# Kernel tuning notes

Measured on AMD Instinct MI355X. Metric: run time of the kernel, lower is better.

The kernel has to match this reference:

```python
import jax, jax.numpy as jnp
import numpy as np

N = 100000       # num nodes
E = 3200000      # num edges
F_IN = 32        # num_node_features
F_EDGE = 16      # num_edge_features
H = 27           # hidden_dim
OUT = 1          # output_dim


def setup_inputs() -> dict:
    key = jax.random.key(0)
    ks = jax.random.split(key, 12)
    inp = {
        "x": jax.random.normal(ks[0], (N, F_IN), dtype=jnp.float32),
        "edge_index": jax.random.randint(ks[1], (2, E), 0, N, dtype=jnp.int64),
        "edge_attr": jax.random.normal(ks[2], (E, F_EDGE), dtype=jnp.float32),
        # GCNConv layer params (PyG uses weight [in, out] applied as x @ W)
        "W1": jax.random.normal(ks[3], (F_IN, H), dtype=jnp.float32) * (1.0 / np.sqrt(F_IN)),
        "b1": jnp.zeros((H,), dtype=jnp.float32),
        "W2": jax.random.normal(ks[4], (H, H), dtype=jnp.float32) * (1.0 / np.sqrt(H)),
        "b2": jnp.zeros((H,), dtype=jnp.float32),
        # edge MLP
        "ew1": jax.random.normal(ks[5], (F_EDGE, H), dtype=jnp.float32) * (1.0 / np.sqrt(F_EDGE)),
        "eb1": jnp.zeros((H,), dtype=jnp.float32),
        "ew2": jax.random.normal(ks[6], (H, H), dtype=jnp.float32) * (1.0 / np.sqrt(H)),
        "eb2": jnp.zeros((H,), dtype=jnp.float32),
        # final edge head: in = 2*H + H = 3*H
        "fcw": jax.random.normal(ks[7], (3 * H, OUT), dtype=jnp.float32) * (1.0 / np.sqrt(3 * H)),
        "fcb": jnp.zeros((OUT,), dtype=jnp.float32),
    }
    return inp


def gcn_conv(x, edge_index, W, b):
    # PyG GCNConv with add_self_loops=True, symmetric normalization.
    row, col = edge_index[0], edge_index[1]
    loops = jnp.arange(N, dtype=edge_index.dtype)
    row_sl = jnp.concatenate([row, loops])  # sources
    col_sl = jnp.concatenate([col, loops])  # targets
    # degree computed on target nodes (edge weights = 1)
    deg = jax.ops.segment_sum(jnp.ones_like(col_sl, dtype=x.dtype), col_sl, num_segments=N)
    dinv = jnp.where(deg > 0, jax.lax.rsqrt(deg), 0.0)
    norm = dinv[row_sl] * dinv[col_sl]  # [E+N]
    h = x @ W  # [N, H]
    msg = h[row_sl] * norm[:, None]  # gather + scale
    out = jax.ops.segment_sum(msg, col_sl, num_segments=N)  # scatter-add
    return out + b


def reference(x, edge_index, edge_attr, W1, b1, W2, b2, ew1, eb1, ew2, eb2, fcw, fcb):
    h = jax.nn.relu(gcn_conv(x, edge_index, W1, b1))
    # dropout is identity in eval mode (training=False)
    h = gcn_conv(h, edge_index, W2, b2)
    ef = jax.nn.relu(edge_attr @ ew1 + eb1) @ ew2 + eb2  # [E, H]
    row, col = edge_index[0], edge_index[1]
    emb = jnp.concatenate([h[row], h[col], ef], axis=1)  # [E, 3H]
    pred = (emb @ fcw + fcb).squeeze()  # [E]
    return pred
```

## Files before the change

kernel.cpp:

```cpp
#include <hip/hip_runtime.h>

#define N_NODES 100000
#define N_EDGES 3200000
#define F_IN 32
#define F_EDGE 16
#define H 27
#define PAD 32
#define NB_NODES 391
#define NBUCK 391
#define BCAP 9216
#define CHUNK 12500

__global__ __launch_bounds__(256) void k_initcur(int* __restrict__ cursor) {
    int i = blockIdx.x * 256 + threadIdx.x;
    if (i < NBUCK) cursor[i] = i * BCAP;
}

__global__ __launch_bounds__(1024) void k_bin(const int* __restrict__ ei,
                                              int* __restrict__ cursor,
                                              int* __restrict__ binned) {
    __shared__ int stage[CHUNK];
    __shared__ int hist[NBUCK];
    __shared__ int bstart[NBUCK];
    __shared__ int gbase[NBUCK];
    __shared__ int scanbuf[512];
    int tid = threadIdx.x;
    long long cs = (long long)blockIdx.x * CHUNK;

    for (int i = tid; i < NBUCK; i += 1024) hist[i] = 0;
    __syncthreads();

    int pk[13], bk[13], rk[13];
#pragma unroll
    for (int i = 0; i < 13; i++) {
        int j = tid + i * 1024;
        bk[i] = -1;
        if (j < CHUNK) {
            int e = (int)(cs + j);
            int r = ei[e];
            int c = ei[N_EDGES + e];
            int b = c >> 8;
            pk[i] = (r << 8) | (c & 255);
            bk[i] = b;
            rk[i] = atomicAdd(&hist[b], 1);
        }
    }
    __syncthreads();

    if (tid < 512) scanbuf[tid] = (tid < NBUCK) ? hist[tid] : 0;
    __syncthreads();
    for (int off = 1; off < 512; off <<= 1) {
        int v = 0;
        if (tid < 512 && tid >= off) v = scanbuf[tid - off];
        __syncthreads();
        if (tid < 512) scanbuf[tid] += v;
        __syncthreads();
    }
    if (tid < NBUCK) {
        bstart[tid] = scanbuf[tid] - hist[tid];
        gbase[tid] = (hist[tid] > 0) ? atomicAdd(&cursor[tid], hist[tid]) : 0;
    }
    __syncthreads();

#pragma unroll
    for (int i = 0; i < 13; i++) {
        if (bk[i] >= 0) stage[bstart[bk[i]] + rk[i]] = pk[i];
    }
    __syncthreads();

    for (int j = tid; j < CHUNK; j += 1024) {
        int lo = 0, hi = NBUCK - 1;
        while (lo < hi) {
            int mid = (lo + hi + 1) >> 1;
            if (bstart[mid] <= j) lo = mid; else hi = mid - 1;
        }
        binned[gbase[lo] + (j - bstart[lo])] = stage[j];
    }
}

__global__ __launch_bounds__(512) void k_bscan(const int* __restrict__ cursor,
                                               int* __restrict__ bbase,
                                               int* __restrict__ ptr) {
    __shared__ int sb[512];
    int tid = threadIdx.x;
    int cnt = (tid < NBUCK) ? (cursor[tid] - tid * BCAP) : 0;
    sb[tid] = cnt;
    __syncthreads();
    for (int off = 1; off < 512; off <<= 1) {
        int t = (tid >= off) ? sb[tid - off] : 0;
        __syncthreads();
        sb[tid] += t;
        __syncthreads();
    }
    if (tid < NBUCK) bbase[tid] = sb[tid] - cnt;
    if (tid == NBUCK - 1) ptr[N_NODES] = sb[tid];
}

__global__ __launch_bounds__(256) void k_bin2(const int* __restrict__ cursor,
                                              const int* __restrict__ binned,
                                              const int* __restrict__ bbase,
                                              int* __restrict__ ptr,
                                              int* __restrict__ csr,
                                              float* __restrict__ dinv) {
    __shared__ int hist[256];
    __shared__ int offs[256];
    __shared__ int stage[BCAP];
    int b = blockIdx.x, tid = threadIdx.x;
    hist[tid] = 0;
    __syncthreads();
    int base = b * BCAP;
    int cnt = cursor[b] - base;
    int gb = bbase[b];

    int recs[36], rks[36];
#pragma unroll
    for (int i = 0; i < 36; i++) {
        int j = tid + i * 256;
        recs[i] = -1;
        if (j < cnt) {
            int rec = binned[base + j];
            recs[i] = rec;
            rks[i] = atomicAdd(&hist[rec & 255], 1);
        }
    }
    __syncthreads();

    int v = hist[tid];
    offs[tid] = v;
    __syncthreads();
    for (int off = 1; off < 256; off <<= 1) {
        int t = (tid >= off) ? offs[tid - off] : 0;
        __syncthreads();
        offs[tid] += t;
        __syncthreads();
    }
    int excl = offs[tid] - v;
    int n = b * 256 + tid;
    if (n < N_NODES) {
        ptr[n] = gb + excl;
        dinv[n] = rsqrtf((float)(v + 1));
    }
    __syncthreads();
    offs[tid] = excl;
    __syncthreads();

#pragma unroll
    for (int i = 0; i < 36; i++) {
        if (recs[i] >= 0) stage[offs[recs[i] & 255] + rks[i]] = recs[i] >> 8;
    }
    __syncthreads();
    for (int j = tid; j < cnt; j += 256) csr[gb + j] = stage[j];
}

__global__ __launch_bounds__(256) void k_l1pre(const float* __restrict__ x,
                                               const float* __restrict__ W1,
                                               const float* __restrict__ dinv,
                                               float* __restrict__ bufA) {
    __shared__ float w[F_IN * H];
    for (int i = threadIdx.x; i < F_IN * H; i += 256) w[i] = W1[i];
    __syncthreads();
    int n = blockIdx.x * 256 + threadIdx.x;
    if (n >= N_NODES) return;

    float xv[F_IN];
    const float4* xp = (const float4*)(x + (long long)n * F_IN);
#pragma unroll
    for (int j = 0; j < F_IN / 4; j++) {
        float4 v = xp[j];
        xv[4 * j] = v.x; xv[4 * j + 1] = v.y; xv[4 * j + 2] = v.z; xv[4 * j + 3] = v.w;
    }
    float di = dinv[n];
    long long base = (long long)n * PAD;
#pragma unroll
    for (int j = 0; j < H; j++) {
        float acc = 0.f;
#pragma unroll
        for (int k = 0; k < F_IN; k++) acc += xv[k] * w[k * H + j];
        bufA[base + j] = acc * di;
    }
}

__global__ __launch_bounds__(256) void k_gather_post(const int* __restrict__ ptr,
                                                     const int* __restrict__ csr,
                                                     const float* __restrict__ bufA,
                                                     const float* __restrict__ W2,
                                                     const float* __restrict__ b1,
                                                     const float* __restrict__ fcw,
                                                     const float* __restrict__ dinv,
                                                     float2* __restrict__ s01) {
    __shared__ float w[H * H];
    __shared__ float bs[H], f0[H], f1[H];
    for (int i = threadIdx.x; i < H * H; i += 256) w[i] = W2[i];
    if (threadIdx.x < H) {
        bs[threadIdx.x] = b1[threadIdx.x];
        f0[threadIdx.x] = fcw[threadIdx.x];
        f1[threadIdx.x] = fcw[H + threadIdx.x];
    }
    __syncthreads();

    int g = blockIdx.x * 256 + threadIdx.x;
    int n = g >> 5;
    int lane = g & 31;
    if (n >= N_NODES) return;
    int sub = lane >> 3;
    int q = lane & 7;
    int p0 = ptr[n], p1 = ptr[n + 1];

    float4 a0 = make_float4(0.f, 0.f, 0.f, 0.f);
    float4 a1 = make_float4(0.f, 0.f, 0.f, 0.f);
    int i = p0;
    while (i < p1) {
        int m = p1 - i; if (m > 32) m = 32;
        int idx = (lane < m) ? csr[i + lane] : 0;
        for (int jj = 0; jj < m; jj += 8) {
            int e0 = jj + sub;
            int e1 = jj + 4 + sub;
            int r0 = __shfl(idx, e0, 32);
            int r1 = __shfl(idx, e1, 32);
            float4 v0 = ((const float4*)(bufA + (long long)r0 * PAD))[q];
            float4 v1 = ((const float4*)(bufA + (long long)r1 * PAD))[q];
            if (e0 < m) { a0.x += v0.x; a0.y += v0.y; a0.z += v0.z; a0.w += v0.w; }
            if (e1 < m) { a1.x += v1.x; a1.y += v1.y; a1.z += v1.z; a1.w += v1.w; }
        }
        i += m;
    }
    a0.x += a1.x; a0.y += a1.y; a0.z += a1.z; a0.w += a1.w;

    a0.x += __shfl_xor(a0.x, 8, 32);
    a0.y += __shfl_xor(a0.y, 8, 32);
    a0.z += __shfl_xor(a0.z, 8, 32);
    a0.w += __shfl_xor(a0.w, 8, 32);
    a0.x += __shfl_xor(a0.x, 16, 32);
    a0.y += __shfl_xor(a0.y, 16, 32);
    a0.z += __shfl_xor(a0.z, 16, 32);
    a0.w += __shfl_xor(a0.w, 16, 32);

    float4 sv = ((const float4*)(bufA + (long long)n * PAD))[q];
    a0.x += sv.x; a0.y += sv.y; a0.z += sv.z; a0.w += sv.w;

    int src = lane >> 2;
    float t0 = __shfl(a0.x, src, 32);
    float t1 = __shfl(a0.y, src, 32);
    float t2 = __shfl(a0.z, src, 32);
    float t3 = __shfl(a0.w, src, 32);
    int c = lane & 3;
    float acc = (c == 0) ? t0 : (c == 1) ? t1 : (c == 2) ? t2 : t3;

    float di = dinv[n];
    float o1 = 0.f;
    if (lane < H) {
        float t = bs[lane] + di * acc;
        o1 = t > 0.f ? t : 0.f;
    }
    float gj = 0.f;
#pragma unroll
    for (int k = 0; k < H; k++) {
        float ok = __shfl(o1, k, 32);
        if (lane < H) gj += ok * w[k * H + lane];
    }
    float t0h = 0.f, t1h = 0.f;
    if (lane < H) {
        float gd = gj * di;
        t0h = gd * f0[lane];
        t1h = gd * f1[lane];
    }
#pragma unroll
    for (int off = 16; off > 0; off >>= 1) {
        t0h += __shfl_xor(t0h, off, 32);
        t1h += __shfl_xor(t1h, off, 32);
    }
    if (lane == 0) s01[n] = make_float2(t0h, t1h);
}

__global__ void k_prep(const float* __restrict__ ew2,
                       const float* __restrict__ eb2,
                       const float* __restrict__ b2,
                       const float* __restrict__ fcw,
                       const float* __restrict__ fcb,
                       float* __restrict__ vbuf) {
    int k = threadIdx.x;
    if (k < H) {
        float acc = 0.f;
#pragma unroll
        for (int j = 0; j < H; j++) acc += ew2[k * H + j] * fcw[2 * H + j];
        vbuf[k] = acc;
    } else if (k == H) {
        float acc = fcb[0];
#pragma unroll
        for (int j = 0; j < H; j++) acc += eb2[j] * fcw[2 * H + j];
        vbuf[H] = acc;
    } else if (k == H + 1) {
        float acc = 0.f;
#pragma unroll
        for (int j = 0; j < H; j++) acc += b2[j] * fcw[j];
        vbuf[H + 1] = acc;
    } else if (k == H + 2) {
        float acc = 0.f;
#pragma unroll
        for (int j = 0; j < H; j++) acc += b2[j] * fcw[H + j];
        vbuf[H + 2] = acc;
    }
}

__global__ __launch_bounds__(256) void k_pull2(const int* __restrict__ ptr,
                                               const int* __restrict__ csr,
                                               const float2* __restrict__ s01,
                                               const float* __restrict__ dinv,
                                               const float* __restrict__ vbuf,
                                               float* __restrict__ pr,
                                               float* __restrict__ pc) {
    int g = blockIdx.x * 256 + threadIdx.x;
    int n = g >> 5;
    int lane = g & 31;
    if (n >= N_NODES) return;
    int p0 = ptr[n], p1 = ptr[n + 1];

    float a0 = 0.f, a1 = 0.f;
    for (int i = p0 + lane; i < p1; i += 32) {
        float2 s = s01[csr[i]];
        a0 += s.x;
        a1 += s.y;
    }
#pragma unroll
    for (int off = 16; off > 0; off >>= 1) {
        a0 += __shfl_down(a0, off, 32);
        a1 += __shfl_down(a1, off, 32);
    }
    if (lane == 0) {
        float2 ss = s01[n];
        float di = dinv[n];
        pr[n] = vbuf[H + 1] + di * (a0 + ss.x);
        pc[n] = vbuf[H + 2] + di * (a1 + ss.y);
    }
}

__global__ __launch_bounds__(256) void k_edge_final(const int* __restrict__ ei,
                                                    const float* __restrict__ ea,
                                                    const float* __restrict__ ew1,
                                                    const float* __restrict__ eb1,
                                                    const float* __restrict__ vbuf,
                                                    const float* __restrict__ pr,
                                                    const float* __restrict__ pc,
                                                    float* __restrict__ out) {
    __shared__ float w1t[H * F_EDGE];
    __shared__ float2 bv[H];
    __shared__ float c0s;
    for (int i = threadIdx.x; i < H * F_EDGE; i += 256) {
        int k = i >> 4, m = i & 15;
        w1t[i] = ew1[m * H + k];
    }
    if (threadIdx.x < H) bv[threadIdx.x] = make_float2(eb1[threadIdx.x], vbuf[threadIdx.x]);
    if (threadIdx.x == 0) c0s = vbuf[H];
    __syncthreads();

    long long t = (long long)blockIdx.x * 256 + threadIdx.x;
    long long e0 = t * 2;
    if (e0 >= N_EDGES) return;

    int2 rr = *(const int2*)(ei + e0);
    int2 cc = *(const int2*)(ei + N_EDGES + e0);
    float g0 = pr[rr.x];
    float g1 = pr[rr.y];
    float h0 = pc[cc.x];
    float h1 = pc[cc.y];

    float a[2][F_EDGE];
#pragma unroll
    for (int i = 0; i < 2; i++) {
        const float4* p = (const float4*)(ea + (e0 + i) * F_EDGE);
#pragma unroll
        for (int j = 0; j < F_EDGE / 4; j++) {
            float4 v = p[j];
            a[i][4 * j] = v.x; a[i][4 * j + 1] = v.y; a[i][4 * j + 2] = v.z; a[i][4 * j + 3] = v.w;
        }
    }

    float c0 = c0s;
    float acc0 = c0, acc1 = c0;
    const float4* w1v = (const float4*)w1t;
#pragma unroll
    for (int k = 0; k < H; k++) {
        float4 wa = w1v[k * 4 + 0];
        float4 wb = w1v[k * 4 + 1];
        float4 wc = w1v[k * 4 + 2];
        float4 wd = w1v[k * 4 + 3];
        float2 bvk = bv[k];
        float s0 = bvk.x;
        s0 += a[0][0] * wa.x + a[0][1] * wa.y + a[0][2] * wa.z + a[0][3] * wa.w;
        s0 += a[0][4] * wb.x + a[0][5] * wb.y + a[0][6] * wb.z + a[0][7] * wb.w;
        s0 += a[0][8] * wc.x + a[0][9] * wc.y + a[0][10] * wc.z + a[0][11] * wc.w;
        s0 += a[0][12] * wd.x + a[0][13] * wd.y + a[0][14] * wd.z + a[0][15] * wd.w;
        float s1 = bvk.x;
        s1 += a[1][0] * wa.x + a[1][1] * wa.y + a[1][2] * wa.z + a[1][3] * wa.w;
        s1 += a[1][4] * wb.x + a[1][5] * wb.y + a[1][6] * wb.z + a[1][7] * wb.w;
        s1 += a[1][8] * wc.x + a[1][9] * wc.y + a[1][10] * wc.z + a[1][11] * wc.w;
        s1 += a[1][12] * wd.x + a[1][13] * wd.y + a[1][14] * wd.z + a[1][15] * wd.w;
        acc0 += (s0 > 0.f ? s0 : 0.f) * bvk.y;
        acc1 += (s1 > 0.f ? s1 : 0.f) * bvk.y;
    }

    acc0 += g0 + h0;
    acc1 += g1 + h1;
    *(float2*)(out + e0) = make_float2(acc0, acc1);
}

extern "C" void kernel_launch(void* const* d_in, const int* in_sizes, int n_in,
                              void* d_out, int out_size, void* d_ws, size_t ws_size,
                              hipStream_t stream) {
    const float* x   = (const float*)d_in[0];
    const int*   ei  = (const int*)d_in[1];
    const float* ea  = (const float*)d_in[2];
    const float* W1  = (const float*)d_in[3];
    const float* b1  = (const float*)d_in[4];
    const float* W2  = (const float*)d_in[5];
    const float* b2  = (const float*)d_in[6];
    const float* ew1 = (const float*)d_in[7];
    const float* eb1 = (const float*)d_in[8];
    const float* ew2 = (const float*)d_in[9];
    const float* eb2 = (const float*)d_in[10];
    const float* fcw = (const float*)d_in[11];
    const float* fcb = (const float*)d_in[12];
    float* out = (float*)d_out;

    int* cursor  = (int*)d_ws;
    int* bbase   = cursor + 1024;
    int* binned  = bbase + 512;
    int* ptr     = binned + (size_t)NBUCK * BCAP;
    int* csr     = ptr + N_NODES + 1024;
    float* dinv  = (float*)(csr + N_EDGES);
    float* bufA  = dinv + N_NODES;
    float2* s01  = (float2*)(bufA + (size_t)N_NODES * PAD);
    float* pr    = (float*)(s01 + N_NODES);
    float* pc    = pr + N_NODES;
    float* vbuf  = pc + N_NODES;

    const int nb_ng = (N_NODES * 32 + 255) / 256;
    const int nb_e2 = N_EDGES / 2 / 256;

    k_initcur<<<2, 256, 0, stream>>>(cursor);
    k_bin<<<256, 1024, 0, stream>>>(ei, cursor, binned);
    k_bscan<<<1, 512, 0, stream>>>(cursor, bbase, ptr);
    k_bin2<<<NBUCK, 256, 0, stream>>>(cursor, binned, bbase, ptr, csr, dinv);

    k_prep<<<1, 64, 0, stream>>>(ew2, eb2, b2, fcw, fcb, vbuf);

    k_l1pre<<<NB_NODES, 256, 0, stream>>>(x, W1, dinv, bufA);
    k_gather_post<<<nb_ng, 256, 0, stream>>>(ptr, csr, bufA, W2, b1, fcw, dinv, s01);

    k_pull2<<<nb_ng, 256, 0, stream>>>(ptr, csr, s01, dinv, vbuf, pr, pc);

    k_edge_final<<<nb_e2, 256, 0, stream>>>(ei, ea, ew1, eb1, vbuf, pr, pc, out);
}
```

Baseline: 481.5 us.

## Merge cursor init into prep, warp-per-bucket binned copy, vectorize bufA stores

Three changes. The separate cursor-init kernel is folded into k_prep, which now runs with 512 threads first, removing one launch. In k_bin, the per-element binary search over bucket starts is replaced by a loop where each 32-lane group copies whole buckets contiguously, which removes the search cost and makes writes coalesced. k_l1pre now writes each padded row as float4 stores with zeroed padding instead of 27 scalar stores. Short buckets leave lanes idle in the new copy loop.

```diff
diff --git a/kernel.cpp b/kernel.cpp
--- a/kernel.cpp
+++ b/kernel.cpp
@@ -10,11 +10,6 @@
 #define NBUCK 391
 #define BCAP 9216
 #define CHUNK 12500
-
-__global__ __launch_bounds__(256) void k_initcur(int* __restrict__ cursor) {
-    int i = blockIdx.x * 256 + threadIdx.x;
-    if (i < NBUCK) cursor[i] = i * BCAP;
-}
 
 __global__ __launch_bounds__(1024) void k_bin(const int* __restrict__ ei,
                                               int* __restrict__ cursor,
@@ -68,13 +63,15 @@
     }
     __syncthreads();
 
-    for (int j = tid; j < CHUNK; j += 1024) {
-        int lo = 0, hi = NBUCK - 1;
-        while (lo < hi) {
-            int mid = (lo + hi + 1) >> 1;
-            if (bstart[mid] <= j) lo = mid; else hi = mid - 1;
-        }
-        binned[gbase[lo] + (j - bstart[lo])] = stage[j];
+    int lane = tid & 31;
+    int grp = tid >> 5;
+    for (int b = grp; b < NBUCK; b += 32) {
+        int cnt = hist[b];
+        if (cnt == 0) continue;
+        int s = bstart[b];
+        int g = gbase[b];
+        for (int l = lane; l < cnt; l += 32)
+            binned[g + l] = stage[s + l];
     }
 }
 
@@ -170,14 +167,20 @@
         xv[4 * j] = v.x; xv[4 * j + 1] = v.y; xv[4 * j + 2] = v.z; xv[4 * j + 3] = v.w;
     }
     float di = dinv[n];
-    long long base = (long long)n * PAD;
+    float ov[PAD];
 #pragma unroll
     for (int j = 0; j < H; j++) {
         float acc = 0.f;
 #pragma unroll
         for (int k = 0; k < F_IN; k++) acc += xv[k] * w[k * H + j];
-        bufA[base + j] = acc * di;
-    }
+        ov[j] = acc * di;
+    }
+#pragma unroll
+    for (int j = H; j < PAD; j++) ov[j] = 0.f;
+    float4* op = (float4*)(bufA + (long long)n * PAD);
+#pragma unroll
+    for (int j = 0; j < PAD / 4; j++)
+        op[j] = make_float4(ov[4 * j], ov[4 * j + 1], ov[4 * j + 2], ov[4 * j + 3]);
 }
 
 __global__ __launch_bounds__(256) void k_gather_post(const int* __restrict__ ptr,
@@ -272,13 +275,15 @@
     if (lane == 0) s01[n] = make_float2(t0h, t1h);
 }
 
-__global__ void k_prep(const float* __restrict__ ew2,
-                       const float* __restrict__ eb2,
-                       const float* __restrict__ b2,
-                       const float* __restrict__ fcw,
-                       const float* __restrict__ fcb,
-                       float* __restrict__ vbuf) {
+__global__ __launch_bounds__(512) void k_prep(const float* __restrict__ ew2,
+                                              const float* __restrict__ eb2,
+                                              const float* __restrict__ b2,
+                                              const float* __restrict__ fcw,
+                                              const float* __restrict__ fcb,
+                                              float* __restrict__ vbuf,
+                                              int* __restrict__ cursor) {
     int k = threadIdx.x;
+    if (k < NBUCK) cursor[k] = k * BCAP;
     if (k < H) {
         float acc = 0.f;
 #pragma unroll
@@ -437,13 +442,12 @@
     const int nb_ng = (N_NODES * 32 + 255) / 256;
     const int nb_e2 = N_EDGES / 2 / 256;
 
-    k_initcur<<<2, 256, 0, stream>>>(cursor);
+    k_prep<<<1, 512, 0, stream>>>(ew2, eb2, b2, fcw, fcb, vbuf, cursor);
+
     k_bin<<<256, 1024, 0, stream>>>(ei, cursor, binned);
     k_bscan<<<1, 512, 0, stream>>>(cursor, bbase, ptr);
     k_bin2<<<NBUCK, 256, 0, stream>>>(cursor, binned, bbase, ptr, csr, dinv);
 
-    k_prep<<<1, 64, 0, stream>>>(ew2, eb2, b2, fcw, fcb, vbuf);
-
     k_l1pre<<<NB_NODES, 256, 0, stream>>>(x, W1, dinv, bufA);
     k_gather_post<<<nb_ng, 256, 0, stream>>>(ptr, csr, bufA, W2, b1, fcw, dinv, s01);
 
```

Result: no change. 474.5 us, median of 2 (-1.5%).
